# Kernel optimization log

Hardware: AMD Instinct MI355X
Metric: run time of the kernel (lower is better)

The kernel has to match this reference:

```python
import jax, jax.numpy as jnp
import numpy as np
import math

TOP_K = 3
LN_EPS = 1e-5


def _conv2d(x, w, b):
    # x: (1, C_in, T, p), w: (C_out, C_in, 3, 3) OIHW, padding=1 -> SAME
    y = jax.lax.conv_general_dilated(
        x, w, window_strides=(1, 1), padding=[(1, 1), (1, 1)],
        dimension_numbers=('NCHW', 'OIHW', 'NCHW'))
    return y + b[None, :, None, None]


def _dominant_periods(x, top_k):
    # fft over channel-mean series, drop DC, take top-k frequency indices + 1
    fft_vals = jnp.abs(jnp.fft.rfft(x.mean(-1), axis=-1))  # (B, L//2+1)
    fft_vals = fft_vals.at[:, 0].set(0.0)
    idx = jax.lax.top_k(fft_vals, top_k)[1] + 1  # (B, top_k)
    return np.asarray(idx)  # concrete ints: periods are data-dependent shapes


def setup_inputs() -> dict:
    key = jax.random.key(0)
    ks = jax.random.split(key, 3)
    B, L, D, C = 64, 1024, 256, 128
    return {
        'x': jax.random.normal(ks[0], (B, L, D), jnp.float32),
        'W1': jax.random.normal(ks[1], (C, D, 3, 3), jnp.float32) * 0.02,
        'b1': jnp.zeros((C,), jnp.float32),
        'W2': jax.random.normal(ks[2], (D, C, 3, 3), jnp.float32) * 0.02,
        'b2': jnp.zeros((D,), jnp.float32),
        'gamma': jnp.ones((D,), jnp.float32),
        'beta': jnp.zeros((D,), jnp.float32),
    }


def reference(x, W1, b1, W2, b2, gamma, beta):
    B, L, D = x.shape
    periods = _dominant_periods(x, TOP_K)  # (B, TOP_K) concrete
    outs = []
    for bi in range(B):
        acc = jnp.zeros((L, D), x.dtype)
        for p in periods[bi]:
            p = int(p)
            if p <= 1:
                continue
            T = math.ceil(L / p)
            pad = T * p - L
            # (D, L) -> pad -> (1, D, T, p)
            xi = jnp.pad(x[bi].T, ((0, 0), (0, pad))).reshape(1, D, T, p)
            xi = _conv2d(xi, W1, b1)
            xi = jax.nn.gelu(xi, approximate=False)  # torch GELU is exact
            xi = _conv2d(xi, W2, b2)
            xi = xi.reshape(1, D, T * p)[..., :L]
            acc = acc + xi[0].T
        outs.append(acc)
    out = jnp.stack(outs) / TOP_K
    y = x + out
    mu = y.mean(-1, keepdims=True)
    var = y.var(-1, keepdims=True)
    yn = (y - mu) * jax.lax.rsqrt(var + LN_EPS)
    return yn * gamma + beta
```

## Files before the change

kernel.cpp:

```cpp
#include <hip/hip_runtime.h>
#include <hip/hip_bf16.h>
#include <math.h>

#define B_ 64
#define L_ 1024
#define D_ 256
#define C_ 128
#define LPMAX 1536

typedef __bf16 bf16x8 __attribute__((ext_vector_type(8)));
typedef float f32x16 __attribute__((ext_vector_type(16)));

__device__ __forceinline__ unsigned short f2bf(float f) {
    __hip_bfloat16 h = __float2bfloat16(f);
    return __builtin_bit_cast(unsigned short, h);
}

__device__ __forceinline__ float gelu_exact(float f) {
    return 0.5f * f * (1.0f + erff(f * 0.70710678118654752440f));
}

__device__ __forceinline__ void gl16(const unsigned short* g, unsigned short* l) {
    __builtin_amdgcn_global_load_lds(
        (const __attribute__((address_space(1))) unsigned int*)g,
        (__attribute__((address_space(3))) unsigned int*)l, 16, 0, 0);
}

__global__ void prep_kernel(const float* __restrict__ x, unsigned short* __restrict__ xb,
                            float* __restrict__ series) {
    int row = blockIdx.x * 4 + (threadIdx.x >> 6);
    int lane = threadIdx.x & 63;
    size_t base = (size_t)row * D_ + lane * 4;
    float4 v = *reinterpret_cast<const float4*>(x + base);
    ushort4 o;
    o.x = f2bf(v.x); o.y = f2bf(v.y); o.z = f2bf(v.z); o.w = f2bf(v.w);
    *reinterpret_cast<ushort4*>(xb + base) = o;
    float s = v.x + v.y + v.z + v.w;
    #pragma unroll
    for (int d = 32; d; d >>= 1) s += __shfl_xor(s, d);
    if (lane == 0) series[row] = s * (1.0f / D_);
}

__global__ void tw_kernel(double* __restrict__ tw) {
    int j = blockIdx.x * 256 + threadIdx.x;
    if (j < 1024) {
        double a = -2.0 * 3.14159265358979323846 * (double)j / 1024.0;
        tw[2 * j] = cos(a);
        tw[2 * j + 1] = sin(a);
    }
}

__global__ void repack_kernel(const float* __restrict__ W1, const float* __restrict__ W2,
                              unsigned short* __restrict__ W1s, unsigned short* __restrict__ W2s) {
    int i = blockIdx.x * 256 + threadIdx.x;
    if (i < 294912) {
        int img = i >> 12;
        int tap = img >> 3, kk = img & 7;
        int within = i & 4095;
        int rb = within >> 9, q = (within >> 7) & 3, rr = (within >> 3) & 15, e = i & 7;
        int c = rb * 16 + rr, d = kk * 32 + q * 8 + e;
        int dt = tap / 3, dp = tap % 3;
        W1s[i] = f2bf(W1[((c * D_ + d) * 3 + dt) * 3 + dp]);
    } else {
        int i2 = i - 294912;
        if (i2 < 294912) {
            int img = i2 >> 13;
            int tap = img >> 2, kk = img & 3;
            int within = i2 & 8191;
            int rb = within >> 9, q = (within >> 7) & 3, rr = (within >> 3) & 15, e = i2 & 7;
            int dout = rb * 16 + rr, cin = kk * 32 + q * 8 + e;
            int dt = tap / 3, dp = tap % 3;
            W2s[i2] = f2bf(W2[((dout * C_ + cin) * 3 + dt) * 3 + dp]);
        }
    }
}

__global__ void dft_kernel(const float* __restrict__ series, const double* __restrict__ tw,
                           float* __restrict__ mag2) {
    int bk = blockIdx.x;
    int k = bk % 513, b = bk / 513;
    int lane = threadIdx.x;
    const float* s = series + (size_t)b * L_;
    double re = 0.0, im = 0.0;
    #pragma unroll 4
    for (int i = 0; i < 16; i++) {
        int l = lane + 64 * i;
        int idx = (k * l) & 1023;
        double sv = (double)s[l];
        re += sv * tw[2 * idx];
        im += sv * tw[2 * idx + 1];
    }
    #pragma unroll
    for (int d = 32; d; d >>= 1) { re += __shfl_down(re, d); im += __shfl_down(im, d); }
    if (lane == 0) mag2[bk] = (k == 0) ? 0.0f : (float)(re * re + im * im);
}

__global__ void topk_kernel(const float* __restrict__ mag2, int* __restrict__ periods) {
    int b = blockIdx.x;
    int lane = threadIdx.x;
    const float* m = mag2 + b * 513;
    float v[9]; int kid[9];
    #pragma unroll
    for (int r = 0; r < 9; r++) {
        int k = r * 64 + lane;
        kid[r] = k;
        v[r] = (k < 513) ? m[k] : -1.0f;
    }
    int s0 = -1, s1 = -1;
    for (int j = 0; j < 3; j++) {
        float best = -1.0f; int bi = 0x7fffffff;
        #pragma unroll
        for (int r = 0; r < 9; r++) {
            bool skip = (kid[r] == s0) || (kid[r] == s1) || (kid[r] >= 513);
            if (!skip && (v[r] > best || (v[r] == best && kid[r] < bi))) { best = v[r]; bi = kid[r]; }
        }
        #pragma unroll
        for (int d = 32; d; d >>= 1) {
            float ov = __shfl_xor(best, d);
            int oi = __shfl_xor(bi, d);
            if (ov > best || (ov == best && oi < bi)) { best = ov; bi = oi; }
        }
        if (lane == 0) periods[b * 3 + j] = bi + 1;
        if (j == 0) s0 = bi; else if (j == 1) s1 = bi;
    }
}

__global__ __launch_bounds__(256, 3)
void conv1_kernel(const unsigned short* __restrict__ xb,
                  const unsigned short* __restrict__ W1s,
                  const float* __restrict__ b1,
                  const int* __restrict__ periods,
                  unsigned short* __restrict__ out1g) {
    __shared__ __align__(16) unsigned short sA[12288];
    __shared__ __align__(16) unsigned short sB[2][5632];

    const int blk = blockIdx.x;
    const int xcd = blk & 7;
    const int li = blk >> 3;
    const int b = xcd * 8 + li / 36;
    const int rem = li % 36;
    const int j = rem / 12, tile = rem % 12;

    const int p = periods[b * 3 + j];
    if (p <= 1) return;
    const int T = (L_ + p - 1) / p;
    const int Lp = T * p;
    const int col0 = tile * 128;
    if (col0 >= Lp) return;

    const int tid = threadIdx.x;
    const int w = tid >> 6, lane = tid & 63;
    const int wm = w >> 1, wn = w & 1;
    const int l15 = lane & 15, l4 = lane >> 4;
    const int l31 = lane & 31, lh = lane >> 5;
    const int s0w = (w < 2) ? w * 3 : 6 + (w - 2) * 2;
    const int nsw = (w < 2) ? 3 : 2;

    const unsigned short* xbb = xb + (size_t)b * L_ * D_;

    int cols2[2], ppv2[2], ttv2[2];
    #pragma unroll
    for (int ci = 0; ci < 2; ci++) {
        cols2[ci] = col0 + wn * 64 + ci * 32 + l31;
        ppv2[ci] = cols2[ci] % p;
        ttv2[ci] = cols2[ci] / p;
    }

    int arow32[2];
    #pragma unroll
    for (int ri = 0; ri < 2; ri++)
        arow32[ri] = (wm * 4 + ri * 2 + (l31 >> 4)) * 512 + lh * 128 + (l31 & 15) * 8;
    const int zoff32 = 10 * 512 + lh * 128 + (l31 & 15) * 8;

    f32x16 acc00 = {0.f}, acc01 = {0.f}, acc10 = {0.f}, acc11 = {0.f};

    {
        int bf = tid >> 7, r = tid & 127;
        ushort4 z = {0, 0, 0, 0};
        *reinterpret_cast<ushort4*>(&sB[bf][10 * 512 + r * 4]) = z;
    }

    int locv[3][2];
    auto setmask = [&](int dt) {
        #pragma unroll
        for (int dp = 0; dp < 3; dp++)
            #pragma unroll
            for (int ci = 0; ci < 2; ci++) {
                int pd = ppv2[ci] + dp, td = ttv2[ci] + dt;
                int t = cols2[ci] + (dt - 1) * p + dp - 1;
                bool ok = (pd >= 1) && (pd <= p) && (td >= 1) && (td <= T) &&
                          (cols2[ci] < Lp) && (t < L_);
                int rc = wn * 64 + ci * 32 + 15 + dp + l31;
                int off = (rc >> 4) * 512 + lh * 128 + (rc & 15) * 8;
                locv[dp][ci] = ok ? off : zoff32;
            }
    };

    const unsigned short* gaB[3];
    auto setaddrB = [&](int dt) {
        const int win1 = col0 + (dt - 1) * p - 16;
        #pragma unroll
        for (int i = 0; i < 3; i++) {
            int c = win1 + (s0w + i) * 16 + l15;
            c = c < 0 ? 0 : (c > L_ - 1 ? L_ - 1 : c);
            gaB[i] = xbb + (size_t)c * D_ + l4 * 8;
        }
    };

    auto stageB = [&](int buf, int kk) {
        unsigned short* lb = sB[buf];
        #pragma unroll
        for (int i = 0; i < 3; i++)
            if (i < nsw) gl16(gaB[i] + kk * 32, lb + (s0w + i) * 512);
    };

    auto stageA = [&](int dt, int kk) {
        #pragma unroll
        for (int s6 = 0; s6 < 6; s6++) {
            int pi = w * 6 + s6;
            int dp = pi >> 3, sub = pi & 7;
            gl16(W1s + (size_t)((dt * 3 + dp) * 8 + kk) * 4096 + sub * 512 + lane * 8,
                 sA + pi * 512);
        }
    };

    setmask(0);
    setaddrB(0);
    stageB(0, 0);
    stageA(0, 0);
    asm volatile("s_waitcnt lgkmcnt(0)" ::: "memory");

    for (int ph = 0; ph < 24; ph++) {
        const int cur = ph & 1;
        const int pn = ph + 1;
        asm volatile("s_waitcnt vmcnt(0)" ::: "memory");
        __builtin_amdgcn_s_barrier();
        __builtin_amdgcn_sched_barrier(0);
        if (pn < 24) {
            if ((pn & 7) == 0) setaddrB(pn >> 3);
            stageB(cur ^ 1, pn & 7);
        }
        __builtin_amdgcn_sched_barrier(0);
        __builtin_amdgcn_s_setprio(1);
        {
            const unsigned short* lb = sB[cur];
            #pragma unroll
            for (int dp = 0; dp < 3; dp++) {
                #pragma unroll
                for (int ks = 0; ks < 2; ks++) {
                    bf16x8 Af0 = *reinterpret_cast<const bf16x8*>(sA + dp * 4096 + arow32[0] + ks * 256);
                    bf16x8 Af1 = *reinterpret_cast<const bf16x8*>(sA + dp * 4096 + arow32[1] + ks * 256);
                    bf16x8 Bf0 = *reinterpret_cast<const bf16x8*>(lb + locv[dp][0] + ks * 256);
                    bf16x8 Bf1 = *reinterpret_cast<const bf16x8*>(lb + locv[dp][1] + ks * 256);
                    acc00 = __builtin_amdgcn_mfma_f32_32x32x16_bf16(Af0, Bf0, acc00, 0, 0, 0);
                    acc01 = __builtin_amdgcn_mfma_f32_32x32x16_bf16(Af0, Bf1, acc01, 0, 0, 0);
                    acc10 = __builtin_amdgcn_mfma_f32_32x32x16_bf16(Af1, Bf0, acc10, 0, 0, 0);
                    acc11 = __builtin_amdgcn_mfma_f32_32x32x16_bf16(Af1, Bf1, acc11, 0, 0, 0);
                }
            }
        }
        __builtin_amdgcn_s_setprio(0);
        asm volatile("s_waitcnt lgkmcnt(0)" ::: "memory");
        __builtin_amdgcn_sched_barrier(0);
        __builtin_amdgcn_s_barrier();
        if (pn < 24) {
            stageA(pn >> 3, pn & 7);
            if ((pn & 7) == 0) setmask(pn >> 3);
        }
    }

    const size_t ob = (size_t)(b * 3 + j) * LPMAX * C_;
    const f32x16* accs[4] = { &acc00, &acc01, &acc10, &acc11 };
    #pragma unroll
    for (int ri = 0; ri < 2; ri++) {
        #pragma unroll
        for (int ci = 0; ci < 2; ci++) {
            const f32x16& a = *accs[ri * 2 + ci];
            const int c = cols2[ci];
            if (c < Lp) {
                #pragma unroll
                for (int t = 0; t < 4; t++) {
                    const int ch = wm * 64 + ri * 32 + t * 8 + 4 * lh;
                    const float4 bias = *reinterpret_cast<const float4*>(b1 + ch);
                    ushort4 o;
                    o.x = f2bf(gelu_exact(a[t * 4 + 0] + bias.x));
                    o.y = f2bf(gelu_exact(a[t * 4 + 1] + bias.y));
                    o.z = f2bf(gelu_exact(a[t * 4 + 2] + bias.z));
                    o.w = f2bf(gelu_exact(a[t * 4 + 3] + bias.w));
                    *reinterpret_cast<ushort4*>(out1g + ob + (size_t)c * C_ + ch) = o;
                }
            }
        }
    }
}

__global__ __launch_bounds__(256, 3)
void conv2_kernel(const unsigned short* __restrict__ out1g,
                  const unsigned short* __restrict__ W2s,
                  const float* __restrict__ b2,
                  const int* __restrict__ periods,
                  const float* __restrict__ x,
                  float* __restrict__ yout) {
    __shared__ __align__(16) unsigned short sA[12288];
    __shared__ __align__(16) unsigned short sB[2][5632];

    const int blk = blockIdx.x;
    const int xcd = blk & 7;
    const int li = blk >> 3;
    const int b = xcd * 8 + (li >> 4);
    const int rem = li & 15;
    const int mh = rem & 1;
    const int tile = rem >> 1;
    const int col0 = tile * 128;

    const int tid = threadIdx.x;
    const int w = tid >> 6, lane = tid & 63;
    const int wm = w >> 1, wn = w & 1;
    const int l15 = lane & 15, l4 = lane >> 4;
    const int l31 = lane & 31, lh = lane >> 5;
    const int s0w = (w < 2) ? w * 3 : 6 + (w - 2) * 2;
    const int nsw = (w < 2) ? 3 : 2;

    int p_all[3];
    #pragma unroll
    for (int jj = 0; jj < 3; jj++) p_all[jj] = periods[b * 3 + jj];
    const int nv = (p_all[0] > 1) + (p_all[1] > 1) + (p_all[2] > 1);

    int cols2[2];
    #pragma unroll
    for (int ci = 0; ci < 2; ci++) cols2[ci] = col0 + wn * 64 + ci * 32 + l31;

    int arow32[2];
    #pragma unroll
    for (int ri = 0; ri < 2; ri++)
        arow32[ri] = (wm * 4 + ri * 2 + (l31 >> 4)) * 512 + lh * 128 + (l31 & 15) * 8;
    const int zoff32 = 10 * 512 + lh * 128 + (l31 & 15) * 8;

    f32x16 acc00 = {0.f}, acc01 = {0.f}, acc10 = {0.f}, acc11 = {0.f};

    {
        int bf = tid >> 7, r = tid & 127;
        ushort4 z = {0, 0, 0, 0};
        *reinterpret_cast<ushort4*>(&sB[bf][10 * 512 + r * 4]) = z;
    }

    int locv[3][2];
    auto setmask = [&](int jn, int dt) {
        const int pj = p_all[jn];
        const int Tj = (L_ + pj - 1) / pj;
        const bool okj = pj > 1;
        #pragma unroll
        for (int dp = 0; dp < 3; dp++)
            #pragma unroll
            for (int ci = 0; ci < 2; ci++) {
                int pv = cols2[ci] % pj, tv = cols2[ci] / pj;
                int pd = pv + dp, td = tv + dt;
                bool ok = okj && (pd >= 1) && (pd <= pj) && (td >= 1) && (td <= Tj);
                int rc = wn * 64 + ci * 32 + 15 + dp + l31;
                int off = (rc >> 4) * 512 + lh * 128 + (rc & 15) * 8;
                locv[dp][ci] = ok ? off : zoff32;
            }
    };

    const unsigned short* gaB[3];
    auto setaddrB = [&](int jn, int dt) {
        const int pj = p_all[jn];
        const unsigned short* bbj = out1g + (size_t)(b * 3 + jn) * LPMAX * C_;
        const int win1 = col0 + (dt - 1) * pj - 16;
        #pragma unroll
        for (int i = 0; i < 3; i++) {
            int c = win1 + (s0w + i) * 16 + l15;
            c = c < 0 ? 0 : (c > LPMAX - 1 ? LPMAX - 1 : c);
            gaB[i] = bbj + (size_t)c * C_ + l4 * 8;
        }
    };

    auto stageB = [&](int buf, int kk) {
        unsigned short* lb = sB[buf];
        #pragma unroll
        for (int i = 0; i < 3; i++)
            if (i < nsw) gl16(gaB[i] + kk * 32, lb + (s0w + i) * 512);
    };

    auto stageA = [&](int dt, int kk) {
        #pragma unroll
        for (int s6 = 0; s6 < 6; s6++) {
            int pi = w * 6 + s6;
            int dp = pi >> 3, sub = pi & 7;
            gl16(W2s + (size_t)((dt * 3 + dp) * 4 + kk) * 8192 + mh * 4096 + sub * 512 + lane * 8,
                 sA + pi * 512);
        }
    };

    setmask(0, 0);
    setaddrB(0, 0);
    stageB(0, 0);
    stageA(0, 0);
    asm volatile("s_waitcnt lgkmcnt(0)" ::: "memory");

    for (int ph = 0; ph < 36; ph++) {
        const int cur = ph & 1;
        const int pn = ph + 1;
        asm volatile("s_waitcnt vmcnt(0)" ::: "memory");
        __builtin_amdgcn_s_barrier();
        __builtin_amdgcn_sched_barrier(0);
        if (pn < 36) {
            if ((pn & 3) == 0) setaddrB(pn / 12, (pn / 4) % 3);
            stageB(cur ^ 1, pn & 3);
        }
        __builtin_amdgcn_sched_barrier(0);
        __builtin_amdgcn_s_setprio(1);
        {
            const unsigned short* lb = sB[cur];
            #pragma unroll
            for (int dp = 0; dp < 3; dp++) {
                #pragma unroll
                for (int ks = 0; ks < 2; ks++) {
                    bf16x8 Af0 = *reinterpret_cast<const bf16x8*>(sA + dp * 4096 + arow32[0] + ks * 256);
                    bf16x8 Af1 = *reinterpret_cast<const bf16x8*>(sA + dp * 4096 + arow32[1] + ks * 256);
                    bf16x8 Bf0 = *reinterpret_cast<const bf16x8*>(lb + locv[dp][0] + ks * 256);
                    bf16x8 Bf1 = *reinterpret_cast<const bf16x8*>(lb + locv[dp][1] + ks * 256);
                    acc00 = __builtin_amdgcn_mfma_f32_32x32x16_bf16(Af0, Bf0, acc00, 0, 0, 0);
                    acc01 = __builtin_amdgcn_mfma_f32_32x32x16_bf16(Af0, Bf1, acc01, 0, 0, 0);
                    acc10 = __builtin_amdgcn_mfma_f32_32x32x16_bf16(Af1, Bf0, acc10, 0, 0, 0);
                    acc11 = __builtin_amdgcn_mfma_f32_32x32x16_bf16(Af1, Bf1, acc11, 0, 0, 0);
                }
            }
        }
        __builtin_amdgcn_s_setprio(0);
        asm volatile("s_waitcnt lgkmcnt(0)" ::: "memory");
        __builtin_amdgcn_sched_barrier(0);
        __builtin_amdgcn_s_barrier();
        if (pn < 36) {
            stageA((pn / 4) % 3, pn & 3);
            if ((pn & 3) == 0) setmask(pn / 12, (pn / 4) % 3);
        }
    }

    const float inv3 = 1.0f / 3.0f;
    const float fnv = (float)nv;
    const f32x16* accs[4] = { &acc00, &acc01, &acc10, &acc11 };
    #pragma unroll
    for (int ri = 0; ri < 2; ri++) {
        #pragma unroll
        for (int ci = 0; ci < 2; ci++) {
            const f32x16& a = *accs[ri * 2 + ci];
            const int c = cols2[ci];
            #pragma unroll
            for (int t = 0; t < 4; t++) {
                const int dout = mh * 128 + wm * 64 + ri * 32 + t * 8 + 4 * lh;
                const float4 bb = *reinterpret_cast<const float4*>(b2 + dout);
                const size_t xoff = ((size_t)b * L_ + c) * D_ + dout;
                const float4 xr = *reinterpret_cast<const float4*>(x + xoff);
                float4 o;
                o.x = xr.x + (a[t * 4 + 0] + fnv * bb.x) * inv3;
                o.y = xr.y + (a[t * 4 + 1] + fnv * bb.y) * inv3;
                o.z = xr.z + (a[t * 4 + 2] + fnv * bb.z) * inv3;
                o.w = xr.w + (a[t * 4 + 3] + fnv * bb.w) * inv3;
                *reinterpret_cast<float4*>(yout + xoff) = o;
            }
        }
    }
}

__global__ void ln_kernel(float* __restrict__ y, const float* __restrict__ gamma,
                          const float* __restrict__ beta) {
    int row = blockIdx.x * 4 + (threadIdx.x >> 6);
    int lane = threadIdx.x & 63;
    size_t base = (size_t)row * D_ + lane * 4;
    float4 v = *reinterpret_cast<const float4*>(y + base);
    float s = v.x + v.y + v.z + v.w;
    float s2 = v.x * v.x + v.y * v.y + v.z * v.z + v.w * v.w;
    #pragma unroll
    for (int d = 32; d; d >>= 1) { s += __shfl_xor(s, d); s2 += __shfl_xor(s2, d); }
    float mu = s * (1.0f / D_);
    float var = s2 * (1.0f / D_) - mu * mu;
    float inv = 1.0f / sqrtf(var + 1e-5f);
    float4 g = *reinterpret_cast<const float4*>(gamma + lane * 4);
    float4 be = *reinterpret_cast<const float4*>(beta + lane * 4);
    float4 o;
    o.x = (v.x - mu) * inv * g.x + be.x;
    o.y = (v.y - mu) * inv * g.y + be.y;
    o.z = (v.z - mu) * inv * g.z + be.z;
    o.w = (v.w - mu) * inv * g.w + be.w;
    *reinterpret_cast<float4*>(y + base) = o;
}

extern "C" void kernel_launch(void* const* d_in, const int* in_sizes, int n_in,
                              void* d_out, int out_size, void* d_ws, size_t ws_size,
                              hipStream_t stream) {
    const float* x     = (const float*)d_in[0];
    const float* W1    = (const float*)d_in[1];
    const float* b1    = (const float*)d_in[2];
    const float* W2    = (const float*)d_in[3];
    const float* b2    = (const float*)d_in[4];
    const float* gamma = (const float*)d_in[5];
    const float* beta  = (const float*)d_in[6];
    float* out = (float*)d_out;

    char* ws = (char*)d_ws;
    size_t off = 0;
    auto walloc = [&](size_t bytes) -> void* {
        void* pp = ws + off;
        off += (bytes + 255) & ~(size_t)255;
        return pp;
    };
    unsigned short* xb    = (unsigned short*)walloc((size_t)B_ * L_ * D_ * 2);
    unsigned short* out1g = (unsigned short*)walloc((size_t)B_ * 3 * LPMAX * C_ * 2);
    float* series         = (float*)walloc((size_t)B_ * L_ * 4);
    float* mag2           = (float*)walloc((size_t)B_ * 513 * 4);
    int* periods          = (int*)walloc((size_t)B_ * 3 * 4);
    double* tw            = (double*)walloc(1024 * 16);
    unsigned short* W1s   = (unsigned short*)walloc((size_t)294912 * 2);
    unsigned short* W2s   = (unsigned short*)walloc((size_t)294912 * 2);

    prep_kernel<<<B_ * L_ / 4, 256, 0, stream>>>(x, xb, series);
    tw_kernel<<<4, 256, 0, stream>>>(tw);
    repack_kernel<<<2304, 256, 0, stream>>>(W1, W2, W1s, W2s);
    dft_kernel<<<B_ * 513, 64, 0, stream>>>(series, tw, mag2);
    topk_kernel<<<B_, 64, 0, stream>>>(mag2, periods);
    conv1_kernel<<<B_ * 3 * 12, 256, 0, stream>>>(xb, W1s, b1, periods, out1g);
    conv2_kernel<<<B_ * 16, 256, 0, stream>>>(out1g, W2s, b2, periods, x, out);
    ln_kernel<<<B_ * L_ / 4, 256, 0, stream>>>(out, gamma, beta);
}
```

Before: 399.6 us.

## Enlarge conv GEMM tiles to 128x256 per block with 4x2 MFMA per wave

Both conv kernels now compute a larger output tile per block. Conv1 spans 256 columns with all 128 channels per wave. Conv2 spans all 256 output channels, so the block no longer splits them into halves. Each wave holds 8 accumulators instead of 4, which improves the MFMA-to-LDS-load ratio and cuts redundant staging of the input windows and the weights. The cost is roughly double the registers and LDS per block, lower occupancy (launch bounds 3 to 2), and half as many blocks. The extra lgkmcnt wait after the prologue is also removed.

```diff
diff --git a/kernel.cpp b/kernel.cpp
--- a/kernel.cpp
+++ b/kernel.cpp
@@ -125,59 +125,64 @@
     }
 }
 
-__global__ __launch_bounds__(256, 3)
+__global__ __launch_bounds__(256, 2)
 void conv1_kernel(const unsigned short* __restrict__ xb,
                   const unsigned short* __restrict__ W1s,
                   const float* __restrict__ b1,
                   const int* __restrict__ periods,
                   unsigned short* __restrict__ out1g) {
     __shared__ __align__(16) unsigned short sA[12288];
-    __shared__ __align__(16) unsigned short sB[2][5632];
+    __shared__ __align__(16) unsigned short sB[2][9728];
 
     const int blk = blockIdx.x;
     const int xcd = blk & 7;
     const int li = blk >> 3;
-    const int b = xcd * 8 + li / 36;
-    const int rem = li % 36;
-    const int j = rem / 12, tile = rem % 12;
+    const int b = xcd * 8 + li / 18;
+    const int rem = li % 18;
+    const int j = rem / 6, tile = rem % 6;
 
     const int p = periods[b * 3 + j];
     if (p <= 1) return;
     const int T = (L_ + p - 1) / p;
     const int Lp = T * p;
-    const int col0 = tile * 128;
+    const int col0 = tile * 256;
     if (col0 >= Lp) return;
 
     const int tid = threadIdx.x;
     const int w = tid >> 6, lane = tid & 63;
-    const int wm = w >> 1, wn = w & 1;
     const int l15 = lane & 15, l4 = lane >> 4;
     const int l31 = lane & 31, lh = lane >> 5;
-    const int s0w = (w < 2) ? w * 3 : 6 + (w - 2) * 2;
-    const int nsw = (w < 2) ? 3 : 2;
+    const int s0w = (w < 2) ? w * 5 : 10 + (w - 2) * 4;
+    const int nsw = (w < 2) ? 5 : 4;
+    const int wcol = w * 64;
 
     const unsigned short* xbb = xb + (size_t)b * L_ * D_;
 
     int cols2[2], ppv2[2], ttv2[2];
     #pragma unroll
     for (int ci = 0; ci < 2; ci++) {
-        cols2[ci] = col0 + wn * 64 + ci * 32 + l31;
+        cols2[ci] = col0 + wcol + ci * 32 + l31;
         ppv2[ci] = cols2[ci] % p;
         ttv2[ci] = cols2[ci] / p;
     }
 
-    int arow32[2];
-    #pragma unroll
-    for (int ri = 0; ri < 2; ri++)
-        arow32[ri] = (wm * 4 + ri * 2 + (l31 >> 4)) * 512 + lh * 128 + (l31 & 15) * 8;
-    const int zoff32 = 10 * 512 + lh * 128 + (l31 & 15) * 8;
-
-    f32x16 acc00 = {0.f}, acc01 = {0.f}, acc10 = {0.f}, acc11 = {0.f};
+    int arow32[4];
+    #pragma unroll
+    for (int ri = 0; ri < 4; ri++)
+        arow32[ri] = (ri * 2 + (l31 >> 4)) * 512 + lh * 128 + (l31 & 15) * 8;
+    const int zoff32 = 18 * 512 + lh * 128 + (l31 & 15) * 8;
+
+    f32x16 acc[4][2];
+    #pragma unroll
+    for (int ri = 0; ri < 4; ri++)
+        #pragma unroll
+        for (int ci = 0; ci < 2; ci++)
+            acc[ri][ci] = f32x16{0.f};
 
     {
         int bf = tid >> 7, r = tid & 127;
         ushort4 z = {0, 0, 0, 0};
-        *reinterpret_cast<ushort4*>(&sB[bf][10 * 512 + r * 4]) = z;
+        *reinterpret_cast<ushort4*>(&sB[bf][18 * 512 + r * 4]) = z;
     }
 
     int locv[3][2];
@@ -190,17 +195,17 @@
                 int t = cols2[ci] + (dt - 1) * p + dp - 1;
                 bool ok = (pd >= 1) && (pd <= p) && (td >= 1) && (td <= T) &&
                           (cols2[ci] < Lp) && (t < L_);
-                int rc = wn * 64 + ci * 32 + 15 + dp + l31;
+                int rc = wcol + ci * 32 + 15 + dp + l31;
                 int off = (rc >> 4) * 512 + lh * 128 + (rc & 15) * 8;
                 locv[dp][ci] = ok ? off : zoff32;
             }
     };
 
-    const unsigned short* gaB[3];
+    const unsigned short* gaB[5];
     auto setaddrB = [&](int dt) {
         const int win1 = col0 + (dt - 1) * p - 16;
         #pragma unroll
-        for (int i = 0; i < 3; i++) {
+        for (int i = 0; i < 5; i++) {
             int c = win1 + (s0w + i) * 16 + l15;
             c = c < 0 ? 0 : (c > L_ - 1 ? L_ - 1 : c);
             gaB[i] = xbb + (size_t)c * D_ + l4 * 8;
@@ -210,7 +215,7 @@
     auto stageB = [&](int buf, int kk) {
         unsigned short* lb = sB[buf];
         #pragma unroll
-        for (int i = 0; i < 3; i++)
+        for (int i = 0; i < 5; i++)
             if (i < nsw) gl16(gaB[i] + kk * 32, lb + (s0w + i) * 512);
     };
 
@@ -228,7 +233,6 @@
     setaddrB(0);
     stageB(0, 0);
     stageA(0, 0);
-    asm volatile("s_waitcnt lgkmcnt(0)" ::: "memory");
 
     for (int ph = 0; ph < 24; ph++) {
         const int cur = ph & 1;
@@ -248,14 +252,14 @@
             for (int dp = 0; dp < 3; dp++) {
                 #pragma unroll
                 for (int ks = 0; ks < 2; ks++) {
-                    bf16x8 Af0 = *reinterpret_cast<const bf16x8*>(sA + dp * 4096 + arow32[0] + ks * 256);
-                    bf16x8 Af1 = *reinterpret_cast<const bf16x8*>(sA + dp * 4096 + arow32[1] + ks * 256);
                     bf16x8 Bf0 = *reinterpret_cast<const bf16x8*>(lb + locv[dp][0] + ks * 256);
                     bf16x8 Bf1 = *reinterpret_cast<const bf16x8*>(lb + locv[dp][1] + ks * 256);
-                    acc00 = __builtin_amdgcn_mfma_f32_32x32x16_bf16(Af0, Bf0, acc00, 0, 0, 0);
-                    acc01 = __builtin_amdgcn_mfma_f32_32x32x16_bf16(Af0, Bf1, acc01, 0, 0, 0);
-                    acc10 = __builtin_amdgcn_mfma_f32_32x32x16_bf16(Af1, Bf0, acc10, 0, 0, 0);
-                    acc11 = __builtin_amdgcn_mfma_f32_32x32x16_bf16(Af1, Bf1, acc11, 0, 0, 0);
+                    #pragma unroll
+                    for (int ri = 0; ri < 4; ri++) {
+                        bf16x8 Af = *reinterpret_cast<const bf16x8*>(sA + dp * 4096 + arow32[ri] + ks * 256);
+                        acc[ri][0] = __builtin_amdgcn_mfma_f32_32x32x16_bf16(Af, Bf0, acc[ri][0], 0, 0, 0);
+                        acc[ri][1] = __builtin_amdgcn_mfma_f32_32x32x16_bf16(Af, Bf1, acc[ri][1], 0, 0, 0);
+                    }
                 }
             }
         }
@@ -270,23 +274,21 @@
     }
 
     const size_t ob = (size_t)(b * 3 + j) * LPMAX * C_;
-    const f32x16* accs[4] = { &acc00, &acc01, &acc10, &acc11 };
-    #pragma unroll
-    for (int ri = 0; ri < 2; ri++) {
+    #pragma unroll
+    for (int ri = 0; ri < 4; ri++) {
         #pragma unroll
         for (int ci = 0; ci < 2; ci++) {
-            const f32x16& a = *accs[ri * 2 + ci];
             const int c = cols2[ci];
             if (c < Lp) {
                 #pragma unroll
                 for (int t = 0; t < 4; t++) {
-                    const int ch = wm * 64 + ri * 32 + t * 8 + 4 * lh;
+                    const int ch = ri * 32 + t * 8 + 4 * lh;
                     const float4 bias = *reinterpret_cast<const float4*>(b1 + ch);
                     ushort4 o;
-                    o.x = f2bf(gelu_exact(a[t * 4 + 0] + bias.x));
-                    o.y = f2bf(gelu_exact(a[t * 4 + 1] + bias.y));
-                    o.z = f2bf(gelu_exact(a[t * 4 + 2] + bias.z));
-                    o.w = f2bf(gelu_exact(a[t * 4 + 3] + bias.w));
+                    o.x = f2bf(gelu_exact(acc[ri][ci][t * 4 + 0] + bias.x));
+                    o.y = f2bf(gelu_exact(acc[ri][ci][t * 4 + 1] + bias.y));
+                    o.z = f2bf(gelu_exact(acc[ri][ci][t * 4 + 2] + bias.z));
+                    o.w = f2bf(gelu_exact(acc[ri][ci][t * 4 + 3] + bias.w));
                     *reinterpret_cast<ushort4*>(out1g + ob + (size_t)c * C_ + ch) = o;
                 }
             }
@@ -294,23 +296,21 @@
     }
 }
 
-__global__ __launch_bounds__(256, 3)
+__global__ __launch_bounds__(256, 2)
 void conv2_kernel(const unsigned short* __restrict__ out1g,
                   const unsigned short* __restrict__ W2s,
                   const float* __restrict__ b2,
                   const int* __restrict__ periods,
                   const float* __restrict__ x,
                   float* __restrict__ yout) {
-    __shared__ __align__(16) unsigned short sA[12288];
+    __shared__ __align__(16) unsigned short sA[24576];
     __shared__ __align__(16) unsigned short sB[2][5632];
 
     const int blk = blockIdx.x;
     const int xcd = blk & 7;
     const int li = blk >> 3;
-    const int b = xcd * 8 + (li >> 4);
-    const int rem = li & 15;
-    const int mh = rem & 1;
-    const int tile = rem >> 1;
+    const int b = xcd * 8 + (li >> 3);
+    const int tile = li & 7;
     const int col0 = tile * 128;
 
     const int tid = threadIdx.x;
@@ -320,6 +320,7 @@
     const int l31 = lane & 31, lh = lane >> 5;
     const int s0w = (w < 2) ? w * 3 : 6 + (w - 2) * 2;
     const int nsw = (w < 2) ? 3 : 2;
+    const int wcol = wn * 64;
 
     int p_all[3];
     #pragma unroll
@@ -328,15 +329,20 @@
 
     int cols2[2];
     #pragma unroll
-    for (int ci = 0; ci < 2; ci++) cols2[ci] = col0 + wn * 64 + ci * 32 + l31;
-
-    int arow32[2];
-    #pragma unroll
-    for (int ri = 0; ri < 2; ri++)
-        arow32[ri] = (wm * 4 + ri * 2 + (l31 >> 4)) * 512 + lh * 128 + (l31 & 15) * 8;
+    for (int ci = 0; ci < 2; ci++) cols2[ci] = col0 + wcol + ci * 32 + l31;
+
+    int arow32[4];
+    #pragma unroll
+    for (int ri = 0; ri < 4; ri++)
+        arow32[ri] = (wm * 8 + ri * 2 + (l31 >> 4)) * 512 + lh * 128 + (l31 & 15) * 8;
     const int zoff32 = 10 * 512 + lh * 128 + (l31 & 15) * 8;
 
-    f32x16 acc00 = {0.f}, acc01 = {0.f}, acc10 = {0.f}, acc11 = {0.f};
+    f32x16 acc[4][2];
+    #pragma unroll
+    for (int ri = 0; ri < 4; ri++)
+        #pragma unroll
+        for (int ci = 0; ci < 2; ci++)
+            acc[ri][ci] = f32x16{0.f};
 
     {
         int bf = tid >> 7, r = tid & 127;
@@ -356,7 +362,7 @@
                 int pv = cols2[ci] % pj, tv = cols2[ci] / pj;
                 int pd = pv + dp, td = tv + dt;
                 bool ok = okj && (pd >= 1) && (pd <= pj) && (td >= 1) && (td <= Tj);
-                int rc = wn * 64 + ci * 32 + 15 + dp + l31;
+                int rc = wcol + ci * 32 + 15 + dp + l31;
                 int off = (rc >> 4) * 512 + lh * 128 + (rc & 15) * 8;
                 locv[dp][ci] = ok ? off : zoff32;
             }
@@ -384,10 +390,10 @@
 
     auto stageA = [&](int dt, int kk) {
         #pragma unroll
-        for (int s6 = 0; s6 < 6; s6++) {
-            int pi = w * 6 + s6;
-            int dp = pi >> 3, sub = pi & 7;
-            gl16(W2s + (size_t)((dt * 3 + dp) * 4 + kk) * 8192 + mh * 4096 + sub * 512 + lane * 8,
+        for (int s12 = 0; s12 < 12; s12++) {
+            int pi = w * 12 + s12;
+            int dp = pi >> 4, sub = pi & 15;
+            gl16(W2s + (size_t)((dt * 3 + dp) * 4 + kk) * 8192 + sub * 512 + lane * 8,
                  sA + pi * 512);
         }
     };
@@ -396,7 +402,6 @@
     setaddrB(0, 0);
     stageB(0, 0);
     stageA(0, 0);
-    asm volatile("s_waitcnt lgkmcnt(0)" ::: "memory");
 
     for (int ph = 0; ph < 36; ph++) {
         const int cur = ph & 1;
@@ -416,14 +421,14 @@
             for (int dp = 0; dp < 3; dp++) {
                 #pragma unroll
                 for (int ks = 0; ks < 2; ks++) {
-                    bf16x8 Af0 = *reinterpret_cast<const bf16x8*>(sA + dp * 4096 + arow32[0] + ks * 256);
-                    bf16x8 Af1 = *reinterpret_cast<const bf16x8*>(sA + dp * 4096 + arow32[1] + ks * 256);
                     bf16x8 Bf0 = *reinterpret_cast<const bf16x8*>(lb + locv[dp][0] + ks * 256);
                     bf16x8 Bf1 = *reinterpret_cast<const bf16x8*>(lb + locv[dp][1] + ks * 256);
-                    acc00 = __builtin_amdgcn_mfma_f32_32x32x16_bf16(Af0, Bf0, acc00, 0, 0, 0);
-                    acc01 = __builtin_amdgcn_mfma_f32_32x32x16_bf16(Af0, Bf1, acc01, 0, 0, 0);
-                    acc10 = __builtin_amdgcn_mfma_f32_32x32x16_bf16(Af1, Bf0, acc10, 0, 0, 0);
-                    acc11 = __builtin_amdgcn_mfma_f32_32x32x16_bf16(Af1, Bf1, acc11, 0, 0, 0);
+                    #pragma unroll
+                    for (int ri = 0; ri < 4; ri++) {
+                        bf16x8 Af = *reinterpret_cast<const bf16x8*>(sA + dp * 8192 + arow32[ri] + ks * 256);
+                        acc[ri][0] = __builtin_amdgcn_mfma_f32_32x32x16_bf16(Af, Bf0, acc[ri][0], 0, 0, 0);
+                        acc[ri][1] = __builtin_amdgcn_mfma_f32_32x32x16_bf16(Af, Bf1, acc[ri][1], 0, 0, 0);
+                    }
                 }
             }
         }
@@ -439,24 +444,22 @@
 
     const float inv3 = 1.0f / 3.0f;
     const float fnv = (float)nv;
-    const f32x16* accs[4] = { &acc00, &acc01, &acc10, &acc11 };
-    #pragma unroll
-    for (int ri = 0; ri < 2; ri++) {
+    #pragma unroll
+    for (int ri = 0; ri < 4; ri++) {
         #pragma unroll
         for (int ci = 0; ci < 2; ci++) {
-            const f32x16& a = *accs[ri * 2 + ci];
             const int c = cols2[ci];
             #pragma unroll
             for (int t = 0; t < 4; t++) {
-                const int dout = mh * 128 + wm * 64 + ri * 32 + t * 8 + 4 * lh;
+                const int dout = wm * 128 + ri * 32 + t * 8 + 4 * lh;
                 const float4 bb = *reinterpret_cast<const float4*>(b2 + dout);
                 const size_t xoff = ((size_t)b * L_ + c) * D_ + dout;
                 const float4 xr = *reinterpret_cast<const float4*>(x + xoff);
                 float4 o;
-                o.x = xr.x + (a[t * 4 + 0] + fnv * bb.x) * inv3;
-                o.y = xr.y + (a[t * 4 + 1] + fnv * bb.y) * inv3;
-                o.z = xr.z + (a[t * 4 + 2] + fnv * bb.z) * inv3;
-                o.w = xr.w + (a[t * 4 + 3] + fnv * bb.w) * inv3;
+                o.x = xr.x + (acc[ri][ci][t * 4 + 0] + fnv * bb.x) * inv3;
+                o.y = xr.y + (acc[ri][ci][t * 4 + 1] + fnv * bb.y) * inv3;
+                o.z = xr.z + (acc[ri][ci][t * 4 + 2] + fnv * bb.z) * inv3;
+                o.w = xr.w + (acc[ri][ci][t * 4 + 3] + fnv * bb.w) * inv3;
                 *reinterpret_cast<float4*>(yout + xoff) = o;
             }
         }
@@ -519,7 +522,7 @@
     repack_kernel<<<2304, 256, 0, stream>>>(W1, W2, W1s, W2s);
     dft_kernel<<<B_ * 513, 64, 0, stream>>>(series, tw, mag2);
     topk_kernel<<<B_, 64, 0, stream>>>(mag2, periods);
-    conv1_kernel<<<B_ * 3 * 12, 256, 0, stream>>>(xb, W1s, b1, periods, out1g);
-    conv2_kernel<<<B_ * 16, 256, 0, stream>>>(out1g, W2s, b2, periods, x, out);
+    conv1_kernel<<<B_ * 3 * 6, 256, 0, stream>>>(xb, W1s, b1, periods, out1g);
+    conv2_kernel<<<B_ * 8, 256, 0, stream>>>(out1g, W2s, b2, periods, x, out);
     ln_kernel<<<B_ * L_ / 4, 256, 0, stream>>>(out, gamma, beta);
 }
```

Measured after the change: 415.9 us. +4.1%, slower.

## Widen conv2 tile to all output channels and fuse LayerNorm epilogue

Applied to the files above, without the earlier changes.

conv2 blocks now cover all 256 output channels per column tile instead of half, doubling the A-tile in LDS and the per-wave accumulators. That removes the duplicated B staging across the two channel halves. With full channel rows resident, LayerNorm is computed in the epilogue through a shuffle and an LDS reduction, which removes the separate ln_kernel and its read and write pass over the output. In exchange the kernel uses more registers and LDS, lowers the occupancy target to 2 blocks, and launches half as many blocks.

```diff
diff --git a/kernel.cpp b/kernel.cpp
--- a/kernel.cpp
+++ b/kernel.cpp
@@ -294,23 +294,23 @@
     }
 }
 
-__global__ __launch_bounds__(256, 3)
+__global__ __launch_bounds__(256, 2)
 void conv2_kernel(const unsigned short* __restrict__ out1g,
                   const unsigned short* __restrict__ W2s,
                   const float* __restrict__ b2,
                   const int* __restrict__ periods,
                   const float* __restrict__ x,
+                  const float* __restrict__ gamma,
+                  const float* __restrict__ beta,
                   float* __restrict__ yout) {
-    __shared__ __align__(16) unsigned short sA[12288];
+    __shared__ __align__(16) unsigned short sA[24576];
     __shared__ __align__(16) unsigned short sB[2][5632];
 
     const int blk = blockIdx.x;
     const int xcd = blk & 7;
     const int li = blk >> 3;
-    const int b = xcd * 8 + (li >> 4);
-    const int rem = li & 15;
-    const int mh = rem & 1;
-    const int tile = rem >> 1;
+    const int b = xcd * 8 + (li >> 3);
+    const int tile = li & 7;
     const int col0 = tile * 128;
 
     const int tid = threadIdx.x;
@@ -320,6 +320,7 @@
     const int l31 = lane & 31, lh = lane >> 5;
     const int s0w = (w < 2) ? w * 3 : 6 + (w - 2) * 2;
     const int nsw = (w < 2) ? 3 : 2;
+    const int wcol = wn * 64;
 
     int p_all[3];
     #pragma unroll
@@ -328,15 +329,20 @@
 
     int cols2[2];
     #pragma unroll
-    for (int ci = 0; ci < 2; ci++) cols2[ci] = col0 + wn * 64 + ci * 32 + l31;
-
-    int arow32[2];
-    #pragma unroll
-    for (int ri = 0; ri < 2; ri++)
-        arow32[ri] = (wm * 4 + ri * 2 + (l31 >> 4)) * 512 + lh * 128 + (l31 & 15) * 8;
+    for (int ci = 0; ci < 2; ci++) cols2[ci] = col0 + wcol + ci * 32 + l31;
+
+    int arow32[4];
+    #pragma unroll
+    for (int ri = 0; ri < 4; ri++)
+        arow32[ri] = (wm * 8 + ri * 2 + (l31 >> 4)) * 512 + lh * 128 + (l31 & 15) * 8;
     const int zoff32 = 10 * 512 + lh * 128 + (l31 & 15) * 8;
 
-    f32x16 acc00 = {0.f}, acc01 = {0.f}, acc10 = {0.f}, acc11 = {0.f};
+    f32x16 acc[4][2];
+    #pragma unroll
+    for (int ri = 0; ri < 4; ri++)
+        #pragma unroll
+        for (int ci = 0; ci < 2; ci++)
+            acc[ri][ci] = f32x16{0.f};
 
     {
         int bf = tid >> 7, r = tid & 127;
@@ -356,7 +362,7 @@
                 int pv = cols2[ci] % pj, tv = cols2[ci] / pj;
                 int pd = pv + dp, td = tv + dt;
                 bool ok = okj && (pd >= 1) && (pd <= pj) && (td >= 1) && (td <= Tj);
-                int rc = wn * 64 + ci * 32 + 15 + dp + l31;
+                int rc = wcol + ci * 32 + 15 + dp + l31;
                 int off = (rc >> 4) * 512 + lh * 128 + (rc & 15) * 8;
                 locv[dp][ci] = ok ? off : zoff32;
             }
@@ -384,10 +390,10 @@
 
     auto stageA = [&](int dt, int kk) {
         #pragma unroll
-        for (int s6 = 0; s6 < 6; s6++) {
-            int pi = w * 6 + s6;
-            int dp = pi >> 3, sub = pi & 7;
-            gl16(W2s + (size_t)((dt * 3 + dp) * 4 + kk) * 8192 + mh * 4096 + sub * 512 + lane * 8,
+        for (int s12 = 0; s12 < 12; s12++) {
+            int pi = w * 12 + s12;
+            int dp = pi >> 4, sub = pi & 15;
+            gl16(W2s + (size_t)((dt * 3 + dp) * 4 + kk) * 8192 + sub * 512 + lane * 8,
                  sA + pi * 512);
         }
     };
@@ -396,7 +402,6 @@
     setaddrB(0, 0);
     stageB(0, 0);
     stageA(0, 0);
-    asm volatile("s_waitcnt lgkmcnt(0)" ::: "memory");
 
     for (int ph = 0; ph < 36; ph++) {
         const int cur = ph & 1;
@@ -416,14 +421,14 @@
             for (int dp = 0; dp < 3; dp++) {
                 #pragma unroll
                 for (int ks = 0; ks < 2; ks++) {
-                    bf16x8 Af0 = *reinterpret_cast<const bf16x8*>(sA + dp * 4096 + arow32[0] + ks * 256);
-                    bf16x8 Af1 = *reinterpret_cast<const bf16x8*>(sA + dp * 4096 + arow32[1] + ks * 256);
                     bf16x8 Bf0 = *reinterpret_cast<const bf16x8*>(lb + locv[dp][0] + ks * 256);
                     bf16x8 Bf1 = *reinterpret_cast<const bf16x8*>(lb + locv[dp][1] + ks * 256);
-                    acc00 = __builtin_amdgcn_mfma_f32_32x32x16_bf16(Af0, Bf0, acc00, 0, 0, 0);
-                    acc01 = __builtin_amdgcn_mfma_f32_32x32x16_bf16(Af0, Bf1, acc01, 0, 0, 0);
-                    acc10 = __builtin_amdgcn_mfma_f32_32x32x16_bf16(Af1, Bf0, acc10, 0, 0, 0);
-                    acc11 = __builtin_amdgcn_mfma_f32_32x32x16_bf16(Af1, Bf1, acc11, 0, 0, 0);
+                    #pragma unroll
+                    for (int ri = 0; ri < 4; ri++) {
+                        bf16x8 Af = *reinterpret_cast<const bf16x8*>(sA + dp * 8192 + arow32[ri] + ks * 256);
+                        acc[ri][0] = __builtin_amdgcn_mfma_f32_32x32x16_bf16(Af, Bf0, acc[ri][0], 0, 0, 0);
+                        acc[ri][1] = __builtin_amdgcn_mfma_f32_32x32x16_bf16(Af, Bf1, acc[ri][1], 0, 0, 0);
+                    }
                 }
             }
         }
@@ -439,51 +444,78 @@
 
     const float inv3 = 1.0f / 3.0f;
     const float fnv = (float)nv;
-    const f32x16* accs[4] = { &acc00, &acc01, &acc10, &acc11 };
-    #pragma unroll
-    for (int ri = 0; ri < 2; ri++) {
+    float sum2[2] = {0.f, 0.f}, ssq2[2] = {0.f, 0.f};
+    #pragma unroll
+    for (int ri = 0; ri < 4; ri++) {
         #pragma unroll
         for (int ci = 0; ci < 2; ci++) {
-            const f32x16& a = *accs[ri * 2 + ci];
             const int c = cols2[ci];
             #pragma unroll
             for (int t = 0; t < 4; t++) {
-                const int dout = mh * 128 + wm * 64 + ri * 32 + t * 8 + 4 * lh;
+                const int dout = wm * 128 + ri * 32 + t * 8 + 4 * lh;
                 const float4 bb = *reinterpret_cast<const float4*>(b2 + dout);
                 const size_t xoff = ((size_t)b * L_ + c) * D_ + dout;
                 const float4 xr = *reinterpret_cast<const float4*>(x + xoff);
+                float y0 = xr.x + (acc[ri][ci][t * 4 + 0] + fnv * bb.x) * inv3;
+                float y1 = xr.y + (acc[ri][ci][t * 4 + 1] + fnv * bb.y) * inv3;
+                float y2 = xr.z + (acc[ri][ci][t * 4 + 2] + fnv * bb.z) * inv3;
+                float y3 = xr.w + (acc[ri][ci][t * 4 + 3] + fnv * bb.w) * inv3;
+                acc[ri][ci][t * 4 + 0] = y0;
+                acc[ri][ci][t * 4 + 1] = y1;
+                acc[ri][ci][t * 4 + 2] = y2;
+                acc[ri][ci][t * 4 + 3] = y3;
+                sum2[ci] += y0 + y1 + y2 + y3;
+                ssq2[ci] += y0 * y0 + y1 * y1 + y2 * y2 + y3 * y3;
+            }
+        }
+    }
+    #pragma unroll
+    for (int ci = 0; ci < 2; ci++) {
+        sum2[ci] += __shfl_xor(sum2[ci], 32);
+        ssq2[ci] += __shfl_xor(ssq2[ci], 32);
+    }
+    float* red = (float*)&sB[0][0];
+    if (lh == 0) {
+        #pragma unroll
+        for (int ci = 0; ci < 2; ci++) {
+            red[((w * 2 + ci) * 32 + l31) * 2 + 0] = sum2[ci];
+            red[((w * 2 + ci) * 32 + l31) * 2 + 1] = ssq2[ci];
+        }
+    }
+    __syncthreads();
+    float muv[2], invv[2];
+    #pragma unroll
+    for (int ci = 0; ci < 2; ci++) {
+        float ts = red[((wn * 2 + ci) * 32 + l31) * 2 + 0] +
+                   red[(((2 + wn) * 2 + ci) * 32 + l31) * 2 + 0];
+        float tq = red[((wn * 2 + ci) * 32 + l31) * 2 + 1] +
+                   red[(((2 + wn) * 2 + ci) * 32 + l31) * 2 + 1];
+        float mu = ts * (1.0f / 256.0f);
+        float var = tq * (1.0f / 256.0f) - mu * mu;
+        muv[ci] = mu;
+        invv[ci] = 1.0f / sqrtf(var + 1e-5f);
+    }
+    #pragma unroll
+    for (int ri = 0; ri < 4; ri++) {
+        #pragma unroll
+        for (int ci = 0; ci < 2; ci++) {
+            const int c = cols2[ci];
+            const float mu = muv[ci], inv = invv[ci];
+            #pragma unroll
+            for (int t = 0; t < 4; t++) {
+                const int dout = wm * 128 + ri * 32 + t * 8 + 4 * lh;
+                const float4 g4 = *reinterpret_cast<const float4*>(gamma + dout);
+                const float4 be4 = *reinterpret_cast<const float4*>(beta + dout);
+                const size_t xoff = ((size_t)b * L_ + c) * D_ + dout;
                 float4 o;
-                o.x = xr.x + (a[t * 4 + 0] + fnv * bb.x) * inv3;
-                o.y = xr.y + (a[t * 4 + 1] + fnv * bb.y) * inv3;
-                o.z = xr.z + (a[t * 4 + 2] + fnv * bb.z) * inv3;
-                o.w = xr.w + (a[t * 4 + 3] + fnv * bb.w) * inv3;
+                o.x = (acc[ri][ci][t * 4 + 0] - mu) * inv * g4.x + be4.x;
+                o.y = (acc[ri][ci][t * 4 + 1] - mu) * inv * g4.y + be4.y;
+                o.z = (acc[ri][ci][t * 4 + 2] - mu) * inv * g4.z + be4.z;
+                o.w = (acc[ri][ci][t * 4 + 3] - mu) * inv * g4.w + be4.w;
                 *reinterpret_cast<float4*>(yout + xoff) = o;
             }
         }
     }
-}
-
-__global__ void ln_kernel(float* __restrict__ y, const float* __restrict__ gamma,
-                          const float* __restrict__ beta) {
-    int row = blockIdx.x * 4 + (threadIdx.x >> 6);
-    int lane = threadIdx.x & 63;
-    size_t base = (size_t)row * D_ + lane * 4;
-    float4 v = *reinterpret_cast<const float4*>(y + base);
-    float s = v.x + v.y + v.z + v.w;
-    float s2 = v.x * v.x + v.y * v.y + v.z * v.z + v.w * v.w;
-    #pragma unroll
-    for (int d = 32; d; d >>= 1) { s += __shfl_xor(s, d); s2 += __shfl_xor(s2, d); }
-    float mu = s * (1.0f / D_);
-    float var = s2 * (1.0f / D_) - mu * mu;
-    float inv = 1.0f / sqrtf(var + 1e-5f);
-    float4 g = *reinterpret_cast<const float4*>(gamma + lane * 4);
-    float4 be = *reinterpret_cast<const float4*>(beta + lane * 4);
-    float4 o;
-    o.x = (v.x - mu) * inv * g.x + be.x;
-    o.y = (v.y - mu) * inv * g.y + be.y;
-    o.z = (v.z - mu) * inv * g.z + be.z;
-    o.w = (v.w - mu) * inv * g.w + be.w;
-    *reinterpret_cast<float4*>(y + base) = o;
 }
 
 extern "C" void kernel_launch(void* const* d_in, const int* in_sizes, int n_in,
@@ -520,6 +552,5 @@
     dft_kernel<<<B_ * 513, 64, 0, stream>>>(series, tw, mag2);
     topk_kernel<<<B_, 64, 0, stream>>>(mag2, periods);
     conv1_kernel<<<B_ * 3 * 12, 256, 0, stream>>>(xb, W1s, b1, periods, out1g);
-    conv2_kernel<<<B_ * 16, 256, 0, stream>>>(out1g, W2s, b2, periods, x, out);
-    ln_kernel<<<B_ * L_ / 4, 256, 0, stream>>>(out, gamma, beta);
-}
+    conv2_kernel<<<B_ * 8, 256, 0, stream>>>(out1g, W2s, b2, periods, x, gamma, beta, out);
+}
```

Measured after the change: 361.9 us. 1.1x faster.
